# Kernel tuning notes

Measured on AMD Instinct MI355X. Metric: run time of the kernel, lower is better.

## Reference

```python
import jax, jax.numpy as jnp
import numpy as np

B, DIM, H, W = 2, 192, 256, 256
WIN = 4
EPS = 1e-5


def _cd_conj(x):
    if len(x) == 1:
        return x
    h = len(x) // 2
    return np.concatenate([_cd_conj(x[:h]), -x[h:]])


def _cd_mult(a, b):
    n = len(a)
    if n == 1:
        return a * b
    h = n // 2
    a1, a2, b1, b2 = a[:h], a[h:], b[:h], b[h:]
    c1 = _cd_mult(a1, b1) - _cd_mult(_cd_conj(b2), a2)
    c2 = _cd_mult(b2, a1) + _cd_mult(a2, _cd_conj(b1))
    return np.concatenate([c1, c2])


def _sedenion_table(n=16):
    # M[i, j, k] = sign s such that e_i * e_j = s * e_k (Cayley-Dickson)
    eye = np.eye(n, dtype=np.float32)
    M = np.zeros((n, n, n), dtype=np.float32)
    for i in range(n):
        for j in range(n):
            M[i, j] = _cd_mult(eye[i], eye[j])
    return M

SED_TABLE = jnp.asarray(_sedenion_table(16))  # (16,16,16)


def layer_norm(x, g, b):
    m = x.mean(-1, keepdims=True)
    v = ((x - m) ** 2).mean(-1, keepdims=True)
    return (x - m) * jax.lax.rsqrt(v + EPS) * g + b


def get_window(x):
    # (B,C,H,W) -> (B,H/4,W/4, s1*s2*C)
    b, c, h, w = x.shape
    x = x.reshape(b, c, h // WIN, WIN, w // WIN, WIN)
    x = x.transpose(0, 2, 4, 3, 5, 1)  # b, h', w', s1, s2, c
    return x.reshape(b, h // WIN, w // WIN, WIN * WIN * c)


def reverse_window(x, c):
    b, hh, ww, _ = x.shape
    x = x.reshape(b, hh, ww, WIN, WIN, c)
    x = x.transpose(0, 5, 1, 3, 2, 4)  # b, c, h', s1, w', s2
    return x.reshape(b, c, hh * WIN, ww * WIN)


def sedenion_full_weight(w_sed):
    # w_sed: (16, dim, dim) component weights -> (16*dim, 16*dim) structured matrix
    d = w_sed.shape[1]
    wf = jnp.einsum('ijk,jde->idke', SED_TABLE, w_sed)
    return wf.reshape(16 * d, 16 * w_sed.shape[2])


def setup_inputs() -> dict:
    key = jax.random.key(0)
    ks = jax.random.split(key, 8)
    d, dh = DIM, 4 * DIM
    s = 0.02
    return {
        'x': jax.random.normal(ks[0], (B, DIM, H, W), jnp.float32),
        'norm1_g': jnp.ones((d,), jnp.float32),
        'norm1_b': jnp.zeros((d,), jnp.float32),
        'w_sed': jax.random.normal(ks[1], (16, d, d), jnp.float32) * s,
        'proj_w': jax.random.normal(ks[2], (d, d), jnp.float32) * s,
        'proj_b': jnp.zeros((d,), jnp.float32),
        'norm2_g': jnp.ones((d,), jnp.float32),
        'norm2_b': jnp.zeros((d,), jnp.float32),
        'fc1_w': jax.random.normal(ks[3], (d, dh), jnp.float32) * s,
        'fc1_b': jnp.zeros((dh,), jnp.float32),
        'fc2_w': jax.random.normal(ks[4], (dh, d), jnp.float32) * s,
        'fc2_b': jnp.zeros((d,), jnp.float32),
    }


def reference(x, norm1_g, norm1_b, w_sed, proj_w, proj_b,
              norm2_g, norm2_b, fc1_w, fc1_b, fc2_w, fc2_b):
    b, c, h, w = x.shape
    # --- attention branch (norm1 -> window -> sedenion linear -> unwindow -> gelu -> proj) ---
    xn = layer_norm(x.transpose(0, 2, 3, 1), norm1_g, norm1_b).transpose(0, 3, 1, 2)
    xw = get_window(xn)                               # (B, H/4, W/4, 16*C)
    wf = sedenion_full_weight(w_sed)                  # (16C, 16C)
    xw = xw @ wf
    x1 = reverse_window(xw, c)                        # (B, C, H, W)
    y = x1.transpose(0, 2, 3, 1)                      # b h w c
    y = jax.nn.gelu(y, approximate=False)
    y = y @ proj_w + proj_b
    x = x + y.transpose(0, 3, 1, 2)
    # --- mlp branch ---
    hbr = layer_norm(x.transpose(0, 2, 3, 1), norm2_g, norm2_b)
    hbr = jax.nn.gelu(hbr @ fc1_w + fc1_b, approximate=False)
    hbr = hbr @ fc2_w + fc2_b
    x = x + hbr.transpose(0, 3, 1, 2)
    return x
```

## Files before the change

kernel.cpp:

```cpp
#include <hip/hip_runtime.h>

typedef short short8 __attribute__((ext_vector_type(8)));
typedef float f32x4 __attribute__((ext_vector_type(4)));

#define DEVINL __device__ __forceinline__

struct SedTab { signed char s[256]; unsigned char j[256]; };

static void cd_mult_host(const float* a, const float* b, float* r, int n) {
    if (n == 1) { r[0] = a[0] * b[0]; return; }
    int h = n / 2;
    float cb1[8], cb2[8], t1[8], t2[8], t3[8], t4[8];
    cb1[0] = b[0]; for (int i = 1; i < h; ++i) cb1[i] = -b[i];
    cb2[0] = b[h]; for (int i = 1; i < h; ++i) cb2[i] = -b[h + i];
    cd_mult_host(a,     b,   t1, h);
    cd_mult_host(cb2,   a+h, t2, h);
    cd_mult_host(b+h,   a,   t3, h);
    cd_mult_host(a+h,   cb1, t4, h);
    for (int i = 0; i < h; ++i) { r[i] = t1[i] - t2[i]; r[h + i] = t3[i] + t4[i]; }
}

static SedTab build_sed() {
    SedTab t{};
    for (int i = 0; i < 16; ++i)
        for (int jj = 0; jj < 16; ++jj) {
            float a[16] = {0}, b[16] = {0}, r[16] = {0};
            a[i] = 1.0f; b[jj] = 1.0f;
            cd_mult_host(a, b, r, 16);
            for (int k = 0; k < 16; ++k)
                if (r[k] != 0.0f) {
                    t.s[i * 16 + k] = (r[k] > 0.f) ? 1 : -1;
                    t.j[i * 16 + k] = (unsigned char)jj;
                }
        }
    return t;
}
static const SedTab g_sed = build_sed();

DEVINL unsigned short f2bf(float v) {
    union { float f; unsigned int u; } c; c.f = v;
    unsigned int r = (c.u + 0x7FFFu + ((c.u >> 16) & 1u)) >> 16;
    return (unsigned short)r;
}
DEVINL float bf2f(unsigned short u) {
    union { unsigned int i; float f; } c; c.i = ((unsigned int)u) << 16; return c.f;
}

DEVINL float gelu_f(float v) {
    float u = 1.5957691216f * (v + 0.044715f * v * v * v);
    return v * __builtin_amdgcn_rcpf(1.0f + __expf(-u));
}

DEVINL void gl2lds16(const void* g, void* l) {
    __builtin_amdgcn_global_load_lds((__attribute__((address_space(1))) const unsigned int*)g,
                                     (__attribute__((address_space(3))) unsigned int*)l, 16, 0, 0);
}

DEVINL int swz(int k, int row) {
    return (k & ~63) | ((((k >> 3) ^ row) & 7) << 3) | (k & 7);
}

__global__ __launch_bounds__(256) void build_wft(const float* __restrict__ w_sed,
                                                 unsigned short* __restrict__ wfT,
                                                 SedTab tab) {
    __shared__ float t[32][33];
    int n0 = blockIdx.y * 32, kk0 = blockIdx.x * 32;
    int k = n0 / 192, i = kk0 / 192;
    int j = tab.j[i * 16 + k];
    float s = (float)tab.s[i * 16 + k];
    int e0 = n0 - k * 192, dd0 = kk0 - i * 192;
    int tx = threadIdx.x & 31, ty = threadIdx.x >> 5;
    const float* base = w_sed + ((size_t)j * 192 + dd0) * 192 + e0;
    for (int it = 0; it < 4; ++it) {
        int row = ty + it * 8;
        t[row][tx] = base[(size_t)row * 192 + tx];
    }
    __syncthreads();
    unsigned short* ob = wfT + (size_t)n0 * 3072 + kk0;
    for (int it = 0; it < 4; ++it) {
        int row = ty + it * 8;
        ob[(size_t)row * 3072 + tx] = f2bf(s * t[tx][row]);
    }
}

__global__ __launch_bounds__(256) void prep_w(const float* __restrict__ proj,
                                              const float* __restrict__ fc1,
                                              const float* __restrict__ fc2,
                                              unsigned short* __restrict__ projT,
                                              unsigned short* __restrict__ fc1T,
                                              unsigned short* __restrict__ fc2T) {
    int t = blockIdx.x * 256 + threadIdx.x;
    if (t < 192 * 192) projT[t] = f2bf(proj[(t % 192) * 192 + t / 192]);
    if (t < 768 * 192) {
        int n = t / 192, k = t % 192;
        fc1T[n * 192 + swz(k, n)] = f2bf(fc1[(size_t)k * 768 + n]);
    }
    if (t < 192 * 768) {
        int o = t / 768, k = t % 768;
        fc2T[o * 768 + swz(k, o)] = f2bf(fc2[(size_t)k * 192 + o]);
    }
}

__global__ __launch_bounds__(256) void ln1_win(const float* __restrict__ x,
                                               const float* __restrict__ g,
                                               const float* __restrict__ bta,
                                               unsigned short* __restrict__ xw,
                                               unsigned short* __restrict__ xwin) {
    __shared__ float vals[192 * 65];
    __shared__ float ps[8][64];
    __shared__ float mrs[2][64];
    int t = threadIdx.x;
    int bid = blockIdx.x;
    int x0 = (bid & 3) << 6;
    int y  = (bid >> 2) & 255;
    int b  = bid >> 10;
    int px = t & 63, cg = t >> 6;
    const float* xp = x + ((size_t)b * 192 * 65536) + (size_t)y * 256 + x0 + px;
    float s = 0.f, s2 = 0.f;
    for (int c = cg; c < 192; c += 4) {
        float v = xp[(size_t)c * 65536];
        vals[c * 65 + px] = v;
        s += v; s2 += v * v;
    }
    ps[cg][px] = s; ps[cg + 4][px] = s2;
    __syncthreads();
    if (t < 64) {
        float S  = ps[0][t] + ps[1][t] + ps[2][t] + ps[3][t];
        float S2 = ps[4][t] + ps[5][t] + ps[6][t] + ps[7][t];
        float mean = S * (1.0f / 192.0f);
        float var  = S2 * (1.0f / 192.0f) - mean * mean;
        mrs[0][t] = mean;
        mrs[1][t] = rsqrtf(var + 1e-5f);
    }
    __syncthreads();
    int wh = y >> 2, wr = y & 3;
    for (int i = t; i < 192 * 64; i += 256) {
        int p = i / 192;
        int c = i - p * 192;
        float v = vals[c * 65 + p];
        int xx = x0 + p;
        int ww = xx >> 2, wc = xx & 3;
        int gp = ((b * 64 + wh) * 64 + ww) * 16 + wr * 4 + wc;
        size_t o = (size_t)gp * 192 + c;
        xwin[o] = f2bf(v);
        xw[o] = f2bf((v - mrs[0][p]) * mrs[1][p] * g[c] + bta[c]);
    }
}

template<int TM, int TN, int EPI>
__global__ __launch_bounds__(256, 2) void gemm_bf16(
        const unsigned short* __restrict__ A, const unsigned short* __restrict__ BT,
        const float* __restrict__ bias, unsigned short* __restrict__ outB,
        unsigned short* __restrict__ xresb,
        const float* __restrict__ g2, const float* __restrict__ b2,
        int K, int N) {
    constexpr int WN = TN / 2;
    constexpr int NT = WN / 16;
    constexpr int MT = TM / 32;
    constexpr int HR = TM / 2;
    __shared__ __align__(16) char smem[(TM * 64 + TN * 64) * 2];
    short* lsA = (short*)smem;
    short* lsB = (short*)(smem + TM * 64 * 2);
    int tid = threadIdx.x, lane = tid & 63, wid = tid >> 6;
    int wrow = wid >> 1, wcol = wid & 1;
    int lm = lane & 15, lq = lane >> 4;
    int bm = blockIdx.x * TM, bn = blockIdx.y * TN;
    const unsigned short* Ag = A + (size_t)bm * K;
    const unsigned short* Bg = BT + (size_t)bn * K;
    f32x4 acc[MT][NT] = {};
    for (int k0 = 0; k0 < K; k0 += 64) {
        #pragma unroll
        for (int it = 0; it < TM / 32; ++it) {
            int p = (it * 4 + wid) * 64 + lane;
            int r = p >> 3;
            int q = (p & 7) ^ (r & 7);
            gl2lds16(Ag + (size_t)r * K + k0 + q * 8, lsA + (it * 4 + wid) * 512);
        }
        #pragma unroll
        for (int it = 0; it < TN / 32; ++it) {
            int p = (it * 4 + wid) * 64 + lane;
            int r = p >> 3;
            int q = (p & 7) ^ (r & 7);
            gl2lds16(Bg + (size_t)r * K + k0 + q * 8, lsB + (it * 4 + wid) * 512);
        }
        __syncthreads();
        #pragma unroll
        for (int s = 0; s < 2; ++s) {
            short8 af[MT], bfr[NT];
            #pragma unroll
            for (int mt = 0; mt < MT; ++mt) {
                int r = wrow * HR + mt * 16 + lm;
                int q = s * 4 + lq;
                int pos = r * 8 + (q ^ (r & 7));
                af[mt] = *(const short8*)&lsA[pos * 8];
            }
            #pragma unroll
            for (int nt = 0; nt < NT; ++nt) {
                int r = wcol * WN + nt * 16 + lm;
                int q = s * 4 + lq;
                int pos = r * 8 + (q ^ (r & 7));
                bfr[nt] = *(const short8*)&lsB[pos * 8];
            }
            #pragma unroll
            for (int mt = 0; mt < MT; ++mt)
                #pragma unroll
                for (int nt = 0; nt < NT; ++nt)
                    acc[mt][nt] = __builtin_amdgcn_mfma_f32_16x16x32_bf16(af[mt], bfr[nt], acc[mt][nt], 0, 0, 0);
        }
        __syncthreads();
    }
    int rowB = bm + wrow * HR + lq * 4;
    int colB = bn + wcol * WN + lm;

    if constexpr (EPI == 0) {
        #pragma unroll
        for (int mt = 0; mt < MT; ++mt)
            #pragma unroll
            for (int nt = 0; nt < NT; ++nt)
                #pragma unroll
                for (int r = 0; r < 4; ++r) {
                    int gr = rowB + mt * 16 + r;
                    int gc = colB + nt * 16;
                    float v = acc[mt][nt][r];
                    if (bias) v += bias[gc];
                    outB[(size_t)gr * N + gc] = f2bf(gelu_f(v));
                }
    } else {
        float sA[MT][4], s2A[MT][4];
        #pragma unroll
        for (int mt = 0; mt < MT; ++mt)
            #pragma unroll
            for (int r = 0; r < 4; ++r) { sA[mt][r] = 0.f; s2A[mt][r] = 0.f; }
        #pragma unroll
        for (int mt = 0; mt < MT; ++mt)
            #pragma unroll
            for (int nt = 0; nt < NT; ++nt)
                #pragma unroll
                for (int r = 0; r < 4; ++r) {
                    int gr = rowB + mt * 16 + r;
                    int gc = colB + nt * 16;
                    size_t o = (size_t)gr * 192 + gc;
                    float v = bf2f(xresb[o]) + acc[mt][nt][r] + bias[gc];
                    xresb[o] = f2bf(v);
                    acc[mt][nt][r] = v;
                    sA[mt][r] += v; s2A[mt][r] += v * v;
                }
        #pragma unroll
        for (int mt = 0; mt < MT; ++mt)
            #pragma unroll
            for (int r = 0; r < 4; ++r)
                #pragma unroll
                for (int msk = 1; msk < 16; msk <<= 1) {
                    sA[mt][r]  += __shfl_xor(sA[mt][r],  msk, 64);
                    s2A[mt][r] += __shfl_xor(s2A[mt][r], msk, 64);
                }
        float* psS   = (float*)smem;
        float* psS2  = psS + 256;
        float* pmean = psS2 + 256;
        float* prsig = pmean + 128;
        if (lm == 0) {
            #pragma unroll
            for (int mt = 0; mt < MT; ++mt)
                #pragma unroll
                for (int r = 0; r < 4; ++r) {
                    int rl = wrow * HR + mt * 16 + lq * 4 + r;
                    psS [rl * 2 + wcol] = sA[mt][r];
                    psS2[rl * 2 + wcol] = s2A[mt][r];
                }
        }
        __syncthreads();
        if (tid < TM) {
            float S  = psS[tid * 2]  + psS[tid * 2 + 1];
            float S2 = psS2[tid * 2] + psS2[tid * 2 + 1];
            float mean = S * (1.0f / 192.0f);
            float var  = S2 * (1.0f / 192.0f) - mean * mean;
            pmean[tid] = mean;
            prsig[tid] = rsqrtf(var + 1e-5f);
        }
        __syncthreads();
        float gw[NT], bw[NT];
        #pragma unroll
        for (int nt = 0; nt < NT; ++nt) {
            int gc = colB + nt * 16;
            gw[nt] = g2[gc]; bw[nt] = b2[gc];
        }
        #pragma unroll
        for (int mt = 0; mt < MT; ++mt)
            #pragma unroll
            for (int nt = 0; nt < NT; ++nt)
                #pragma unroll
                for (int r = 0; r < 4; ++r) {
                    int gr = rowB + mt * 16 + r;
                    int rl = wrow * HR + mt * 16 + lq * 4 + r;
                    int gc = colB + nt * 16;
                    float v = (acc[mt][nt][r] - pmean[rl]) * prsig[rl] * gw[nt] + bw[nt];
                    outB[(size_t)gr * 192 + swz(gc, gr)] = f2bf(v);
                }
    }
}

__global__ __launch_bounds__(512, 2) void ffn_fused(
        const unsigned short* __restrict__ A3, const unsigned short* __restrict__ fc1T,
        const unsigned short* __restrict__ fc2T, const float* __restrict__ b1,
        const float* __restrict__ b2, const unsigned short* __restrict__ xresb,
        float* __restrict__ outF) {
    __shared__ __align__(16) char smem[65536];
    short* wA = (short*)smem;
    short* wB = (short*)(smem + 24576);
    short* Sb = (short*)(smem + 49152);
    int tid = threadIdx.x, lane = tid & 63, wid = tid >> 6;
    int wrow = wid >> 1, wcol = wid & 1;
    int lm = lane & 15, lq = lane >> 4;
    int bm = blockIdx.x * 128;

    const unsigned short* A3g = A3 + (size_t)bm * 192;

    auto stage_fc1 = [&](int slice) {
        const unsigned short* f1g = fc1T + (size_t)slice * 64 * 192;
        #pragma unroll
        for (int it = 0; it < 3; ++it) {
            int cb = it * 512 + wid * 64;
            gl2lds16(f1g + (size_t)(cb + lane) * 8, wA + cb * 8);
        }
    };
    auto stage_fc2 = [&](int slice) {
        int kb = slice * 64;
        #pragma unroll
        for (int it = 0; it < 3; ++it) {
            int cb = it * 512 + wid * 64;
            int ch = cb + lane;
            gl2lds16(fc2T + (size_t)(ch >> 3) * 768 + kb + (ch & 7) * 8, wB + cb * 8);
        }
    };

    stage_fc1(0);
    stage_fc2(0);

    short8 af[6][2];
    #pragma unroll
    for (int ks = 0; ks < 6; ++ks) {
        int c = ks * 4 + lq;
        #pragma unroll
        for (int mt = 0; mt < 2; ++mt) {
            int r = wrow * 32 + mt * 16 + lm;
            int slot = (c & ~7) | ((c ^ r) & 7);
            af[ks][mt] = *(const short8*)&A3g[(size_t)r * 192 + slot * 8];
        }
    }
    __syncthreads();

    f32x4 acc2[2][6] = {};
    for (int nb = 0; nb < 12; ++nb) {
        f32x4 acc1[2][2] = {};
        __builtin_amdgcn_s_setprio(1);
        #pragma unroll
        for (int ks = 0; ks < 6; ++ks) {
            int c = ks * 4 + lq;
            short8 bfr[2];
            #pragma unroll
            for (int nt = 0; nt < 2; ++nt) {
                int n = wcol * 32 + nt * 16 + lm;
                int slot = (c & ~7) | ((c ^ n) & 7);
                bfr[nt] = *(const short8*)&wA[n * 192 + slot * 8];
            }
            #pragma unroll
            for (int mt = 0; mt < 2; ++mt)
                #pragma unroll
                for (int nt = 0; nt < 2; ++nt)
                    acc1[mt][nt] = __builtin_amdgcn_mfma_f32_16x16x32_bf16(af[ks][mt], bfr[nt], acc1[mt][nt], 0, 0, 0);
        }
        __builtin_amdgcn_s_setprio(0);
        #pragma unroll
        for (int nt = 0; nt < 2; ++nt) {
            int cl = wcol * 32 + nt * 16 + lm;
            float bv = b1[nb * 64 + cl];
            #pragma unroll
            for (int mt = 0; mt < 2; ++mt)
                #pragma unroll
                for (int r = 0; r < 4; ++r) {
                    int row = wrow * 32 + mt * 16 + lq * 4 + r;
                    float v = gelu_f(acc1[mt][nt][r] + bv);
                    int slot = ((cl >> 3) ^ row) & 7;
                    Sb[row * 64 + slot * 8 + (cl & 7)] = f2bf(v);
                }
        }
        asm volatile("s_waitcnt vmcnt(0) lgkmcnt(0)" ::: "memory");
        __builtin_amdgcn_sched_barrier(0);
        __builtin_amdgcn_s_barrier();
        __builtin_amdgcn_sched_barrier(0);
        if (nb < 11) stage_fc1(nb + 1);
        __builtin_amdgcn_s_setprio(1);
        #pragma unroll
        for (int ks = 0; ks < 2; ++ks) {
            int c = ks * 4 + lq;
            short8 sf[2], wf[6];
            #pragma unroll
            for (int mt = 0; mt < 2; ++mt) {
                int r = wrow * 32 + mt * 16 + lm;
                int slot = (c ^ r) & 7;
                sf[mt] = *(const short8*)&Sb[r * 64 + slot * 8];
            }
            #pragma unroll
            for (int nt = 0; nt < 6; ++nt) {
                int o = wcol * 96 + nt * 16 + lm;
                int slot = (c ^ o) & 7;
                wf[nt] = *(const short8*)&wB[o * 64 + slot * 8];
            }
            #pragma unroll
            for (int mt = 0; mt < 2; ++mt)
                #pragma unroll
                for (int nt = 0; nt < 6; ++nt)
                    acc2[mt][nt] = __builtin_amdgcn_mfma_f32_16x16x32_bf16(sf[mt], wf[nt], acc2[mt][nt], 0, 0, 0);
        }
        __builtin_amdgcn_s_setprio(0);
        asm volatile("s_waitcnt vmcnt(0) lgkmcnt(0)" ::: "memory");
        __builtin_amdgcn_sched_barrier(0);
        __builtin_amdgcn_s_barrier();
        __builtin_amdgcn_sched_barrier(0);
        if (nb < 11) stage_fc2(nb + 1);
    }
    float* T = (float*)smem;
    #pragma unroll
    for (int pass = 0; pass < 2; ++pass) {
        if ((wrow >> 1) == pass) {
            #pragma unroll
            for (int nt = 0; nt < 6; ++nt) {
                int col = wcol * 96 + nt * 16 + lm;
                float bv = b2[col];
                #pragma unroll
                for (int mt = 0; mt < 2; ++mt)
                    #pragma unroll
                    for (int r = 0; r < 4; ++r) {
                        int row = wrow * 32 + mt * 16 + lq * 4 + r;
                        int rowT = row - pass * 64;
                        float xr = bf2f(xresb[(size_t)(bm + row) * 192 + col]);
                        T[rowT * 201 + col] = acc2[mt][nt][r] + bv + xr;
                    }
            }
        }
        __syncthreads();
        int bmg = bm + pass * 64;
        int b  = bmg >> 16;
        int wh = (bmg >> 10) & 63;
        int ww0 = (bmg >> 4) & 63;
        int ybase = wh * 4, xbase = ww0 * 4;
        for (int idx = tid; idx < 3072; idx += 512) {
            int xq = idx & 3, run = idx >> 2;
            int c = run >> 2, wr = run & 3;
            int p = xq * 16 + wr * 4;
            f32x4 val;
            val[0] = T[(p + 0) * 201 + c];
            val[1] = T[(p + 1) * 201 + c];
            val[2] = T[(p + 2) * 201 + c];
            val[3] = T[(p + 3) * 201 + c];
            size_t o = (((size_t)b * 192 + c) * 256 + (ybase + wr)) * 256 + xbase + xq * 4;
            *(f32x4*)&outF[o] = val;
        }
        __syncthreads();
    }
}

extern "C" void kernel_launch(void* const* d_in, const int* in_sizes, int n_in,
                              void* d_out, int out_size, void* d_ws, size_t ws_size,
                              hipStream_t stream) {
    const float* x      = (const float*)d_in[0];
    const float* n1g    = (const float*)d_in[1];
    const float* n1b    = (const float*)d_in[2];
    const float* w_sed  = (const float*)d_in[3];
    const float* proj_w = (const float*)d_in[4];
    const float* proj_b = (const float*)d_in[5];
    const float* n2g    = (const float*)d_in[6];
    const float* n2b    = (const float*)d_in[7];
    const float* fc1_w  = (const float*)d_in[8];
    const float* fc1_b  = (const float*)d_in[9];
    const float* fc2_w  = (const float*)d_in[10];
    const float* fc2_b  = (const float*)d_in[11];
    float* out = (float*)d_out;

    char* ws = (char*)d_ws;
    unsigned short* wfT   = (unsigned short*)(ws);
    unsigned short* xw    = (unsigned short*)(ws + 18874368);
    unsigned short* A2    = (unsigned short*)(ws + 69206016);
    unsigned short* xresb = (unsigned short*)(ws + 119537664);
    unsigned short* projT = (unsigned short*)(ws + 169869312);
    unsigned short* fc1T  = (unsigned short*)(ws + 169943040);
    unsigned short* fc2T  = (unsigned short*)(ws + 170237952);
    unsigned short* A3    = A2;

    build_wft<<<dim3(96, 96), 256, 0, stream>>>(w_sed, wfT, g_sed);
    prep_w<<<576, 256, 0, stream>>>(proj_w, fc1_w, fc2_w, projT, fc1T, fc2T);
    ln1_win<<<2048, 256, 0, stream>>>(x, n1g, n1b, xw, xresb);

    gemm_bf16<128, 128, 0><<<dim3(64, 24), 256, 0, stream>>>(
        xw, wfT, nullptr, A2, nullptr, nullptr, nullptr, 3072, 3072);
    gemm_bf16<128, 192, 3><<<dim3(1024, 1), 256, 0, stream>>>(
        A2, projT, proj_b, A3, xresb, n2g, n2b, 192, 192);
    ffn_fused<<<1024, 512, 0, stream>>>(A3, fc1T, fc2T, fc1_b, fc2_b, xresb, out);
}
```

Baseline: 602.9 us.

## Fuse sedenion GEMM with projection GEMM and LayerNorm2 epilogue

Merges the large 3072x3072 sedenion GEMM and the 192x192 projection GEMM into one kernel. Each block computes a 128x192 tile (one window position's channel slab), applies GELU into shared memory, then multiplies by the projection weights and runs the residual add plus LayerNorm2 epilogue. This removes the A2 intermediate round-trip through global memory and one kernel launch. In exchange it needs 72KB of shared memory, which may cut occupancy, and uses a 128x192 tile with a larger accumulator footprint.

```diff
diff --git a/kernel.cpp b/kernel.cpp
--- a/kernel.cpp
+++ b/kernel.cpp
@@ -147,37 +147,38 @@
     }
 }
 
-template<int TM, int TN, int EPI>
-__global__ __launch_bounds__(256, 2) void gemm_bf16(
-        const unsigned short* __restrict__ A, const unsigned short* __restrict__ BT,
-        const float* __restrict__ bias, unsigned short* __restrict__ outB,
+__global__ __launch_bounds__(256, 2) void gemm_fused(
+        const unsigned short* __restrict__ A,
+        const unsigned short* __restrict__ BT,
+        const unsigned short* __restrict__ projTw,
+        const float* __restrict__ pbias,
+        unsigned short* __restrict__ outB,
         unsigned short* __restrict__ xresb,
-        const float* __restrict__ g2, const float* __restrict__ b2,
-        int K, int N) {
-    constexpr int WN = TN / 2;
-    constexpr int NT = WN / 16;
-    constexpr int MT = TM / 32;
-    constexpr int HR = TM / 2;
-    __shared__ __align__(16) char smem[(TM * 64 + TN * 64) * 2];
+        const float* __restrict__ g2, const float* __restrict__ b2) {
+    constexpr int K = 3072;
+    __shared__ __align__(16) char smem[73728];
     short* lsA = (short*)smem;
-    short* lsB = (short*)(smem + TM * 64 * 2);
+    short* lsB = (short*)(smem + 16384);
+    short* A2t = (short*)smem;
+    short* lsP = (short*)(smem + 49152);
     int tid = threadIdx.x, lane = tid & 63, wid = tid >> 6;
     int wrow = wid >> 1, wcol = wid & 1;
     int lm = lane & 15, lq = lane >> 4;
-    int bm = blockIdx.x * TM, bn = blockIdx.y * TN;
+    int bm = blockIdx.x * 128;
+    int by = blockIdx.y;
     const unsigned short* Ag = A + (size_t)bm * K;
-    const unsigned short* Bg = BT + (size_t)bn * K;
-    f32x4 acc[MT][NT] = {};
+    const unsigned short* Bg = BT + (size_t)by * 192 * K;
+    f32x4 acc[4][6] = {};
     for (int k0 = 0; k0 < K; k0 += 64) {
         #pragma unroll
-        for (int it = 0; it < TM / 32; ++it) {
+        for (int it = 0; it < 4; ++it) {
             int p = (it * 4 + wid) * 64 + lane;
             int r = p >> 3;
             int q = (p & 7) ^ (r & 7);
             gl2lds16(Ag + (size_t)r * K + k0 + q * 8, lsA + (it * 4 + wid) * 512);
         }
         #pragma unroll
-        for (int it = 0; it < TN / 32; ++it) {
+        for (int it = 0; it < 6; ++it) {
             int p = (it * 4 + wid) * 64 + lane;
             int r = p >> 3;
             int q = (p & 7) ^ (r & 7);
@@ -186,117 +187,150 @@
         __syncthreads();
         #pragma unroll
         for (int s = 0; s < 2; ++s) {
-            short8 af[MT], bfr[NT];
-            #pragma unroll
-            for (int mt = 0; mt < MT; ++mt) {
-                int r = wrow * HR + mt * 16 + lm;
+            short8 af[4], bfr[6];
+            #pragma unroll
+            for (int mt = 0; mt < 4; ++mt) {
+                int r = wrow * 64 + mt * 16 + lm;
                 int q = s * 4 + lq;
                 int pos = r * 8 + (q ^ (r & 7));
                 af[mt] = *(const short8*)&lsA[pos * 8];
             }
             #pragma unroll
-            for (int nt = 0; nt < NT; ++nt) {
-                int r = wcol * WN + nt * 16 + lm;
+            for (int nt = 0; nt < 6; ++nt) {
+                int r = wcol * 96 + nt * 16 + lm;
                 int q = s * 4 + lq;
                 int pos = r * 8 + (q ^ (r & 7));
                 bfr[nt] = *(const short8*)&lsB[pos * 8];
             }
             #pragma unroll
-            for (int mt = 0; mt < MT; ++mt)
+            for (int mt = 0; mt < 4; ++mt)
                 #pragma unroll
-                for (int nt = 0; nt < NT; ++nt)
+                for (int nt = 0; nt < 6; ++nt)
                     acc[mt][nt] = __builtin_amdgcn_mfma_f32_16x16x32_bf16(af[mt], bfr[nt], acc[mt][nt], 0, 0, 0);
         }
         __syncthreads();
     }
-    int rowB = bm + wrow * HR + lq * 4;
-    int colB = bn + wcol * WN + lm;
-
-    if constexpr (EPI == 0) {
-        #pragma unroll
-        for (int mt = 0; mt < MT; ++mt)
-            #pragma unroll
-            for (int nt = 0; nt < NT; ++nt)
+    #pragma unroll
+    for (int mt = 0; mt < 4; ++mt)
+        #pragma unroll
+        for (int nt = 0; nt < 6; ++nt)
+            #pragma unroll
+            for (int r = 0; r < 4; ++r) {
+                int row = wrow * 64 + mt * 16 + lq * 4 + r;
+                int c = wcol * 96 + nt * 16 + lm;
+                A2t[row * 192 + swz(c, row)] = f2bf(gelu_f(acc[mt][nt][r]));
+            }
+    #pragma unroll
+    for (int mt = 0; mt < 4; ++mt)
+        #pragma unroll
+        for (int nt = 0; nt < 6; ++nt)
+            acc[mt][nt] = f32x4{0.f, 0.f, 0.f, 0.f};
+    __syncthreads();
+    for (int k0 = 0; k0 < 192; k0 += 64) {
+        #pragma unroll
+        for (int it = 0; it < 6; ++it) {
+            int p = (it * 4 + wid) * 64 + lane;
+            int r = p >> 3;
+            int q = (p & 7) ^ (r & 7);
+            gl2lds16(projTw + (size_t)r * 192 + k0 + q * 8, lsP + (it * 4 + wid) * 512);
+        }
+        __syncthreads();
+        #pragma unroll
+        for (int s = 0; s < 2; ++s) {
+            short8 af[4], bfr[6];
+            #pragma unroll
+            for (int mt = 0; mt < 4; ++mt) {
+                int r = wrow * 64 + mt * 16 + lm;
+                int cg = (k0 >> 3) + s * 4 + lq;
+                int slot = (cg & ~7) | ((cg ^ r) & 7);
+                af[mt] = *(const short8*)&A2t[r * 192 + slot * 8];
+            }
+            #pragma unroll
+            for (int nt = 0; nt < 6; ++nt) {
+                int r = wcol * 96 + nt * 16 + lm;
+                int q = s * 4 + lq;
+                int pos = r * 8 + (q ^ (r & 7));
+                bfr[nt] = *(const short8*)&lsP[pos * 8];
+            }
+            #pragma unroll
+            for (int mt = 0; mt < 4; ++mt)
                 #pragma unroll
-                for (int r = 0; r < 4; ++r) {
-                    int gr = rowB + mt * 16 + r;
-                    int gc = colB + nt * 16;
-                    float v = acc[mt][nt][r];
-                    if (bias) v += bias[gc];
-                    outB[(size_t)gr * N + gc] = f2bf(gelu_f(v));
-                }
-    } else {
-        float sA[MT][4], s2A[MT][4];
-        #pragma unroll
-        for (int mt = 0; mt < MT; ++mt)
-            #pragma unroll
-            for (int r = 0; r < 4; ++r) { sA[mt][r] = 0.f; s2A[mt][r] = 0.f; }
-        #pragma unroll
-        for (int mt = 0; mt < MT; ++mt)
-            #pragma unroll
-            for (int nt = 0; nt < NT; ++nt)
-                #pragma unroll
-                for (int r = 0; r < 4; ++r) {
-                    int gr = rowB + mt * 16 + r;
-                    int gc = colB + nt * 16;
-                    size_t o = (size_t)gr * 192 + gc;
-                    float v = bf2f(xresb[o]) + acc[mt][nt][r] + bias[gc];
-                    xresb[o] = f2bf(v);
-                    acc[mt][nt][r] = v;
-                    sA[mt][r] += v; s2A[mt][r] += v * v;
-                }
-        #pragma unroll
-        for (int mt = 0; mt < MT; ++mt)
-            #pragma unroll
-            for (int r = 0; r < 4; ++r)
-                #pragma unroll
-                for (int msk = 1; msk < 16; msk <<= 1) {
-                    sA[mt][r]  += __shfl_xor(sA[mt][r],  msk, 64);
-                    s2A[mt][r] += __shfl_xor(s2A[mt][r], msk, 64);
-                }
-        float* psS   = (float*)smem;
-        float* psS2  = psS + 256;
-        float* pmean = psS2 + 256;
-        float* prsig = pmean + 128;
-        if (lm == 0) {
-            #pragma unroll
-            for (int mt = 0; mt < MT; ++mt)
-                #pragma unroll
-                for (int r = 0; r < 4; ++r) {
-                    int rl = wrow * HR + mt * 16 + lq * 4 + r;
-                    psS [rl * 2 + wcol] = sA[mt][r];
-                    psS2[rl * 2 + wcol] = s2A[mt][r];
-                }
+                for (int nt = 0; nt < 6; ++nt)
+                    acc[mt][nt] = __builtin_amdgcn_mfma_f32_16x16x32_bf16(af[mt], bfr[nt], acc[mt][nt], 0, 0, 0);
         }
         __syncthreads();
-        if (tid < TM) {
-            float S  = psS[tid * 2]  + psS[tid * 2 + 1];
-            float S2 = psS2[tid * 2] + psS2[tid * 2 + 1];
-            float mean = S * (1.0f / 192.0f);
-            float var  = S2 * (1.0f / 192.0f) - mean * mean;
-            pmean[tid] = mean;
-            prsig[tid] = rsqrtf(var + 1e-5f);
-        }
-        __syncthreads();
-        float gw[NT], bw[NT];
-        #pragma unroll
-        for (int nt = 0; nt < NT; ++nt) {
-            int gc = colB + nt * 16;
-            gw[nt] = g2[gc]; bw[nt] = b2[gc];
-        }
-        #pragma unroll
-        for (int mt = 0; mt < MT; ++mt)
-            #pragma unroll
-            for (int nt = 0; nt < NT; ++nt)
-                #pragma unroll
-                for (int r = 0; r < 4; ++r) {
-                    int gr = rowB + mt * 16 + r;
-                    int rl = wrow * HR + mt * 16 + lq * 4 + r;
-                    int gc = colB + nt * 16;
-                    float v = (acc[mt][nt][r] - pmean[rl]) * prsig[rl] * gw[nt] + bw[nt];
-                    outB[(size_t)gr * 192 + swz(gc, gr)] = f2bf(v);
-                }
-    }
+    }
+    float sA[4][4], s2A[4][4];
+    #pragma unroll
+    for (int mt = 0; mt < 4; ++mt)
+        #pragma unroll
+        for (int r = 0; r < 4; ++r) { sA[mt][r] = 0.f; s2A[mt][r] = 0.f; }
+    #pragma unroll
+    for (int mt = 0; mt < 4; ++mt)
+        #pragma unroll
+        for (int nt = 0; nt < 6; ++nt)
+            #pragma unroll
+            for (int r = 0; r < 4; ++r) {
+                int rl = wrow * 64 + mt * 16 + lq * 4 + r;
+                int gc = wcol * 96 + nt * 16 + lm;
+                size_t gp = (size_t)(bm + rl) * 16 + by;
+                size_t o = gp * 192 + gc;
+                float v = bf2f(xresb[o]) + acc[mt][nt][r] + pbias[gc];
+                xresb[o] = f2bf(v);
+                acc[mt][nt][r] = v;
+                sA[mt][r] += v; s2A[mt][r] += v * v;
+            }
+    #pragma unroll
+    for (int mt = 0; mt < 4; ++mt)
+        #pragma unroll
+        for (int r = 0; r < 4; ++r)
+            #pragma unroll
+            for (int msk = 1; msk < 16; msk <<= 1) {
+                sA[mt][r]  += __shfl_xor(sA[mt][r],  msk, 64);
+                s2A[mt][r] += __shfl_xor(s2A[mt][r], msk, 64);
+            }
+    float* psS   = (float*)smem;
+    float* psS2  = psS + 256;
+    float* pmean = psS2 + 256;
+    float* prsig = pmean + 128;
+    if (lm == 0) {
+        #pragma unroll
+        for (int mt = 0; mt < 4; ++mt)
+            #pragma unroll
+            for (int r = 0; r < 4; ++r) {
+                int rl = wrow * 64 + mt * 16 + lq * 4 + r;
+                psS [rl * 2 + wcol] = sA[mt][r];
+                psS2[rl * 2 + wcol] = s2A[mt][r];
+            }
+    }
+    __syncthreads();
+    if (tid < 128) {
+        float S  = psS[tid * 2]  + psS[tid * 2 + 1];
+        float S2 = psS2[tid * 2] + psS2[tid * 2 + 1];
+        float mean = S * (1.0f / 192.0f);
+        float var  = S2 * (1.0f / 192.0f) - mean * mean;
+        pmean[tid] = mean;
+        prsig[tid] = rsqrtf(var + 1e-5f);
+    }
+    __syncthreads();
+    float gw[6], bw[6];
+    #pragma unroll
+    for (int nt = 0; nt < 6; ++nt) {
+        int gc = wcol * 96 + nt * 16 + lm;
+        gw[nt] = g2[gc]; bw[nt] = b2[gc];
+    }
+    #pragma unroll
+    for (int mt = 0; mt < 4; ++mt)
+        #pragma unroll
+        for (int nt = 0; nt < 6; ++nt)
+            #pragma unroll
+            for (int r = 0; r < 4; ++r) {
+                int rl = wrow * 64 + mt * 16 + lq * 4 + r;
+                int gc = wcol * 96 + nt * 16 + lm;
+                int gp = (bm + rl) * 16 + by;
+                float v = (acc[mt][nt][r] - pmean[rl]) * prsig[rl] * gw[nt] + bw[nt];
+                outB[(size_t)gp * 192 + swz(gc, gp)] = f2bf(v);
+            }
 }
 
 __global__ __launch_bounds__(512, 2) void ffn_fused(
@@ -480,20 +514,17 @@
     char* ws = (char*)d_ws;
     unsigned short* wfT   = (unsigned short*)(ws);
     unsigned short* xw    = (unsigned short*)(ws + 18874368);
-    unsigned short* A2    = (unsigned short*)(ws + 69206016);
+    unsigned short* A3    = (unsigned short*)(ws + 69206016);
     unsigned short* xresb = (unsigned short*)(ws + 119537664);
     unsigned short* projT = (unsigned short*)(ws + 169869312);
     unsigned short* fc1T  = (unsigned short*)(ws + 169943040);
     unsigned short* fc2T  = (unsigned short*)(ws + 170237952);
-    unsigned short* A3    = A2;
 
     build_wft<<<dim3(96, 96), 256, 0, stream>>>(w_sed, wfT, g_sed);
     prep_w<<<576, 256, 0, stream>>>(proj_w, fc1_w, fc2_w, projT, fc1T, fc2T);
     ln1_win<<<2048, 256, 0, stream>>>(x, n1g, n1b, xw, xresb);
 
-    gemm_bf16<128, 128, 0><<<dim3(64, 24), 256, 0, stream>>>(
-        xw, wfT, nullptr, A2, nullptr, nullptr, nullptr, 3072, 3072);
-    gemm_bf16<128, 192, 3><<<dim3(1024, 1), 256, 0, stream>>>(
-        A2, projT, proj_b, A3, xresb, n2g, n2b, 192, 192);
+    gemm_fused<<<dim3(64, 16), 256, 0, stream>>>(
+        xw, wfT, projT, proj_b, A3, xresb, n2g, n2b);
     ffn_fused<<<1024, 512, 0, stream>>>(A3, fc1T, fc2T, fc1_b, fc2_b, xresb, out);
 }
```

After: 576.2 us. 1.05x faster.
